# Performance work log

Measured on AMD Instinct MI355X. Metric: run time of the kernel, lower is better.

Reference implementation:

```python
import jax, jax.numpy as jnp
import numpy as np

NP_, NT_, D_, E_, EP_, L_, R_ = 100000, 300000, 64, 2000000, 500000, 2, 2


def setup_inputs() -> dict:
    key = jax.random.key(0)
    ks = jax.random.split(key, 12)
    return {
        "emb_playlist": jax.random.normal(ks[0], (NP_, D_), jnp.float32),
        "emb_track": jax.random.normal(ks[1], (NT_, D_), jnp.float32),
        "W_rel": jax.random.normal(ks[2], (L_, R_, D_, D_), jnp.float32) * 0.1,
        "W_root": jax.random.normal(ks[3], (L_, D_, D_), jnp.float32) * 0.1,
        "bias": jnp.zeros((L_, D_), jnp.float32),
        "n_id_playlist": jnp.arange(NP_, dtype=jnp.int32),
        "n_id_track": jnp.arange(NT_, dtype=jnp.int32),
        "edge_pt_src": jax.random.randint(ks[4], (E_,), 0, NP_, jnp.int32),
        "edge_pt_dst": jax.random.randint(ks[5], (E_,), 0, NT_, jnp.int32),
        "edge_tp_src": jax.random.randint(ks[6], (E_,), 0, NT_, jnp.int32),
        "edge_tp_dst": jax.random.randint(ks[7], (E_,), 0, NP_, jnp.int32),
        "ell_pl": jax.random.randint(ks[8], (EP_,), 0, NP_, jnp.int32),
        "ell_tr": jax.random.randint(ks[9], (EP_,), 0, NT_, jnp.int32),
    }


def _hetero_gnn(emb_playlist, emb_track, W_rel, W_root, bias,
                n_id_playlist, n_id_track,
                edge_pt_src, edge_pt_dst, edge_tp_src, edge_tp_dst,
                ell_pl, ell_tr):
    NP = emb_playlist.shape[0]
    NT = emb_track.shape[0]
    L = W_root.shape[0]
    N = NP + NT

    # embedding lookup by n_id (identity here, but faithful gather)
    x_pl = emb_playlist[n_id_playlist]
    x_tr = emb_track[n_id_track]

    # alpha=None -> uniform 1/(L+1); buffer is softmaxed -> still uniform
    weights = jax.nn.softmax(jnp.full((L + 1,), 1.0 / (L + 1), jnp.float32))

    out_pl = x_pl * weights[0]
    out_tr = x_tr * weights[0]

    # homogeneous layout: playlists at [0, NP), tracks at [NP, NP+NT)
    x = jnp.concatenate([x_pl, x_tr], axis=0)
    rel_edges = [
        (edge_pt_src, edge_pt_dst + NP),   # playlist -> track
        (edge_tp_src + NP, edge_tp_dst),   # track -> playlist
    ]

    for i in range(L):
        # RGCNConv: root transform + per-relation mean aggregation
        h = x @ W_root[i] + bias[i]
        for r, (src, dst) in enumerate(rel_edges):
            hr = x @ W_rel[i, r]              # [N, D] transform-then-gather
            msg = hr[src]                     # [E, D]
            ssum = jax.ops.segment_sum(msg, dst, num_segments=N)
            cnt = jax.ops.segment_sum(jnp.ones_like(dst, dtype=x.dtype), dst,
                                      num_segments=N)
            h = h + ssum / jnp.maximum(cnt, 1.0)[:, None]
        x = jax.nn.relu(h)
        out_pl = out_pl + x[:NP] * weights[i + 1]
        out_tr = out_tr + x[NP:] * weights[i + 1]

    # global -> local mapping via searchsorted (faithful happy path)
    ps_idx = jnp.argsort(n_id_playlist)
    ps = n_id_playlist[ps_idx]
    pl_loc = ps_idx[jnp.clip(jnp.searchsorted(ps, ell_pl), 0, NP - 1)]
    ts_idx = jnp.argsort(n_id_track)
    ts = n_id_track[ts_idx]
    tr_loc = ts_idx[jnp.clip(jnp.searchsorted(ts, ell_tr), 0, NT - 1)]

    # dot-product link scores (dropout p=0.0 -> identity)
    return jnp.sum(out_pl[pl_loc] * out_tr[tr_loc], axis=-1)


def reference(emb_playlist, emb_track, W_rel, W_root, bias,
              n_id_playlist, n_id_track,
              edge_pt_src, edge_pt_dst, edge_tp_src, edge_tp_dst,
              ell_pl, ell_tr):
    return _hetero_gnn(emb_playlist, emb_track, W_rel, W_root, bias,
                       n_id_playlist, n_id_track,
                       edge_pt_src, edge_pt_dst, edge_tp_src, edge_tp_dst,
                       ell_pl, ell_tr)
```

## Files before the change

kernel.cpp:

```cpp
#include <hip/hip_runtime.h>
#include <stdint.h>

typedef __attribute__((ext_vector_type(8))) short bf16x8;
typedef __attribute__((ext_vector_type(4))) float f32x4;

#define BN 1024
#define BNSHIFT 10
#define MAXNB 512
#define PTI 8192
#define PTHREADS 1024
#define EPT (PTI / PTHREADS)
#define SL 16
#define SSH 15
#define BINS (BN * SL)

static __device__ __forceinline__ float b2f_lo(uint32_t w) {
  union { uint32_t u; float f; } c; c.u = w << 16; return c.f;
}
static __device__ __forceinline__ float b2f_hi(uint32_t w) {
  union { uint32_t u; float f; } c; c.u = w & 0xffff0000u; return c.f;
}
static __device__ __forceinline__ uint16_t f2b(float f) {
  union { float f; uint32_t u; } c; c.f = f;
  return (uint16_t)((c.u + 0x7fffu + ((c.u >> 16) & 1u)) >> 16);
}
static __device__ __forceinline__ void acc8(float* s, uint4 v) {
  s[0] += b2f_lo(v.x); s[1] += b2f_hi(v.x);
  s[2] += b2f_lo(v.y); s[3] += b2f_hi(v.y);
  s[4] += b2f_lo(v.z); s[5] += b2f_hi(v.z);
  s[6] += b2f_lo(v.w); s[7] += b2f_hi(v.w);
}

__global__ __launch_bounds__(256) void convert_kernel(
    const float* __restrict__ emb_pl, const float* __restrict__ emb_tr,
    uint16_t* __restrict__ xb, int NP, int N) {
  long g = (long)blockIdx.x * 256 + threadIdx.x;
  long base8 = g * 8;
  long total = (long)N * 64;
  if (base8 >= total) return;
  long plEnd = (long)NP * 64;
  const float* src = (base8 < plEnd) ? (emb_pl + base8) : (emb_tr + (base8 - plEnd));
  f32x4 a = *(const f32x4*)src;
  f32x4 b = *(const f32x4*)(src + 4);
  union { uint16_t h[8]; uint4 v; } o;
  o.h[0] = f2b(a.x); o.h[1] = f2b(a.y); o.h[2] = f2b(a.z); o.h[3] = f2b(a.w);
  o.h[4] = f2b(b.x); o.h[5] = f2b(b.y); o.h[6] = f2b(b.z); o.h[7] = f2b(b.w);
  *(uint4*)(xb + base8) = o.v;
}

__global__ __launch_bounds__(256) void bucket_hist_kernel(
    const int* __restrict__ pt_dst, const int* __restrict__ tp_dst,
    int* __restrict__ bucketCount, int E, int NP, int NB) {
  extern __shared__ int hist[];
  int t = threadIdx.x;
  for (int b = t; b < NB; b += 256) hist[b] = 0;
  __syncthreads();
  long total = 2L * E;
  long stride = (long)gridDim.x * 256;
  for (long e = (long)blockIdx.x * 256 + t; e < total; e += stride) {
    int dstG = (e < E) ? (NP + pt_dst[e]) : tp_dst[e - E];
    atomicAdd(&hist[dstG >> BNSHIFT], 1);
  }
  __syncthreads();
  for (int b = t; b < NB; b += 256) {
    int h = hist[b];
    if (h > 0) atomicAdd(&bucketCount[b], h);
  }
}

__global__ __launch_bounds__(1024) void bucket_scan_kernel(
    const int* __restrict__ bucketCount, int* __restrict__ bucketStart,
    int* __restrict__ gCursor, int NB) {
  __shared__ int s[1024];
  int t = threadIdx.x;
  int K = (NB + 1023) >> 10;
  int b0 = t * K;
  int local = 0;
  for (int j = 0; j < K; ++j) {
    int b = b0 + j;
    if (b < NB) local += bucketCount[b];
  }
  int acc = local;
  s[t] = local;
  __syncthreads();
  for (int off = 1; off < 1024; off <<= 1) {
    int u = (t >= off) ? s[t - off] : 0;
    __syncthreads();
    acc += u;
    s[t] = acc;
    __syncthreads();
  }
  int run = acc - local;
  for (int j = 0; j < K; ++j) {
    int b = b0 + j;
    if (b < NB) {
      bucketStart[b] = run;
      gCursor[b] = run;
      run += bucketCount[b];
    }
  }
}

__global__ __launch_bounds__(PTHREADS) void partition_kernel(
    const int* __restrict__ pt_src, const int* __restrict__ pt_dst,
    const int* __restrict__ tp_src, const int* __restrict__ tp_dst,
    int* __restrict__ gCursor, uint32_t* __restrict__ pk,
    int E, int NP, int NB) {
  __shared__ uint64_t buf[PTI];
  __shared__ int hist[MAXNB];
  __shared__ int lstart[MAXNB];
  __shared__ int gbase[MAXNB];
  __shared__ int cur[MAXNB];
  __shared__ int sc[PTHREADS];
  int t = threadIdx.x;
  long total = 2L * E;
  long e0 = (long)blockIdx.x * PTI;
  long rem = total - e0;
  int cnt = (rem < (long)PTI) ? (int)rem : PTI;

  for (int j = t; j < NB; j += PTHREADS) hist[j] = 0;
  __syncthreads();

  int bj[EPT];
  uint32_t pkj[EPT];
#pragma unroll
  for (int j = 0; j < EPT; ++j) {
    int i = j * PTHREADS + t;
    bj[j] = -1;
    if (i < cnt) {
      long e = e0 + i;
      int dstG, src;
      if (e < E) {
        dstG = NP + __builtin_nontemporal_load(&pt_dst[e]);
        src = __builtin_nontemporal_load(&pt_src[e]);
      } else {
        dstG = __builtin_nontemporal_load(&tp_dst[e - E]);
        src = NP + __builtin_nontemporal_load(&tp_src[e - E]);
      }
      int b = dstG >> BNSHIFT;
      bj[j] = b;
      pkj[j] = ((uint32_t)(dstG & (BN - 1)) << 20) | (uint32_t)src;
      atomicAdd(&hist[b], 1);
    }
  }
  __syncthreads();

  int h = (t < NB) ? hist[t] : 0;
  int acc = h;
  sc[t] = h;
  __syncthreads();
  for (int off = 1; off < PTHREADS; off <<= 1) {
    int u = (t >= off) ? sc[t - off] : 0;
    __syncthreads();
    acc += u;
    sc[t] = acc;
    __syncthreads();
  }
  if (t < NB) {
    int ls = acc - h;
    lstart[t] = ls;
    cur[t] = ls;
    gbase[t] = (h > 0) ? atomicAdd(&gCursor[t], h) : 0;
  }
  __syncthreads();

#pragma unroll
  for (int j = 0; j < EPT; ++j) {
    int b = bj[j];
    if (b >= 0) {
      int pos = atomicAdd(&cur[b], 1);
      int gpos = gbase[b] + (pos - lstart[b]);
      buf[pos] = ((uint64_t)(uint32_t)gpos << 32) | (uint64_t)pkj[j];
    }
  }
  __syncthreads();

  for (int i = t; i < cnt; i += PTHREADS) {
    uint64_t e = buf[i];
    pk[(uint32_t)(e >> 32)] = (uint32_t)e;
  }
}

__global__ __launch_bounds__(1024) void local_csr_kernel(
    const int* __restrict__ bucketStart, const int* __restrict__ bucketCount,
    const uint32_t* __restrict__ pk, int* __restrict__ rowptr,
    int* __restrict__ col, int N, int TEtotal) {
  __shared__ int hist[BINS];
  __shared__ int ssum[1024];
  int t = threadIdx.x;
  int b = blockIdx.x;
  for (int j = t; j < BINS; j += 1024) hist[j] = 0;
  __syncthreads();
  int beg = bucketStart[b], num = bucketCount[b];
  for (int i = t; i < num; i += 1024) {
    uint32_t w = pk[beg + i];
    int bin = (int)(((w >> 20) << 4) | ((w & 0xFFFFFu) >> SSH));
    atomicAdd(&hist[bin], 1);
  }
  __syncthreads();
  int b0 = t * 16;
  int local = 0;
#pragma unroll
  for (int j = 0; j < 16; ++j) local += hist[b0 + j];
  int acc = local;
  ssum[t] = local;
  __syncthreads();
  for (int off = 1; off < 1024; off <<= 1) {
    int u = (t >= off) ? ssum[t - off] : 0;
    __syncthreads();
    acc += u;
    ssum[t] = acc;
    __syncthreads();
  }
  int run = acc - local;
  int node0 = (b << BNSHIFT) + t;
  if (node0 < N) rowptr[node0] = beg + run;
#pragma unroll
  for (int j = 0; j < 16; ++j) {
    int h = hist[b0 + j];
    hist[b0 + j] = run;
    run += h;
  }
  __syncthreads();
  for (int i = t; i < num; i += 1024) {
    uint32_t w = pk[beg + i];
    int bin = (int)(((w >> 20) << 4) | ((w & 0xFFFFFu) >> SSH));
    int pos = atomicAdd(&hist[bin], 1);
    col[beg + pos] = (int)(w & 0xFFFFFu);
  }
  if (b == 0 && t == 0) rowptr[N] = TEtotal;
}

__global__ __launch_bounds__(256) void pull_kernel(
    const int* __restrict__ rowptr, const int* __restrict__ col,
    const uint16_t* __restrict__ base, uint16_t* __restrict__ agg, int N) {
  int node = blockIdx.x * 32 + (threadIdx.x >> 3);
  int c = threadIdx.x & 7;
  if (node >= N) return;
  int beg = rowptr[node], end = rowptr[node + 1];
  float s[8] = {0, 0, 0, 0, 0, 0, 0, 0};
  const uint16_t* bp = base + c * 8;
  int i = beg;
  for (; i + 4 <= end; i += 4) {
    int c0 = col[i], c1 = col[i + 1], c2 = col[i + 2], c3 = col[i + 3];
    uint4 v0 = *(const uint4*)(bp + (size_t)c0 * 64);
    uint4 v1 = *(const uint4*)(bp + (size_t)c1 * 64);
    uint4 v2 = *(const uint4*)(bp + (size_t)c2 * 64);
    uint4 v3 = *(const uint4*)(bp + (size_t)c3 * 64);
    acc8(s, v0); acc8(s, v1); acc8(s, v2); acc8(s, v3);
  }
  for (; i < end; ++i)
    acc8(s, *(const uint4*)(bp + (size_t)col[i] * 64));
  int deg = end - beg;
  float inv = 1.0f / (float)(deg > 1 ? deg : 1);
  union { uint16_t h[8]; uint4 v; } o;
#pragma unroll
  for (int j = 0; j < 8; ++j) o.h[j] = f2b(s[j] * inv);
  *(uint4*)(agg + (size_t)node * 64 + c * 8) = o.v;
}

template <bool FUSE>
__global__ __launch_bounds__(256) void transform_kernel(
    const uint16_t* __restrict__ xpl, const uint16_t* __restrict__ xtr,
    const uint16_t* __restrict__ agg,
    const float* __restrict__ Wroot,
    const float* __restrict__ WrelP, const float* __restrict__ WrelT,
    const float* __restrict__ biasrow,
    const float* __restrict__ embP, const float* __restrict__ embT,
    uint16_t* __restrict__ xout, int NP, int NT, int BP) {
  int wave = threadIdx.x >> 6;
  int lane = threadIdx.x & 63;
  int m = lane & 15, q = lane >> 4;

  int wl, nw, ntiles, nodeBase;
  const uint16_t* xbase;
  const float* Wrel;
  const float* embBase;
  if ((int)blockIdx.x < BP) {
    wl = blockIdx.x * 4 + wave; nw = BP * 4; ntiles = NP / 16;
    xbase = xpl; Wrel = WrelP; nodeBase = 0; embBase = embP;
  } else {
    wl = (blockIdx.x - BP) * 4 + wave; nw = (gridDim.x - BP) * 4; ntiles = NT / 16;
    xbase = xtr; Wrel = WrelT; nodeBase = NP; embBase = embT;
  }

  bf16x8 br[2][4], bl[2][4];
  for (int kc = 0; kc < 2; ++kc)
    for (int ct = 0; ct < 4; ++ct) {
      int n = 16 * ct + m;
      int k0 = 32 * kc + 8 * q;
      bf16x8 t0, t1;
      for (int i = 0; i < 8; ++i) {
        t0[i] = (short)f2b(Wroot[(size_t)(k0 + i) * 64 + n]);
        t1[i] = (short)f2b(Wrel[(size_t)(k0 + i) * 64 + n]);
      }
      br[kc][ct] = t0;
      bl[kc][ct] = t1;
    }
  float bv[4];
  for (int ct = 0; ct < 4; ++ct) bv[ct] = biasrow[16 * ct + m];

  for (int t = wl; t < ntiles; t += nw) {
    int rowLocal = t * 16 + m;
    int nodeG = nodeBase + rowLocal;
    const uint16_t* xrow = xbase + (size_t)rowLocal * 64;
    bf16x8 ax0 = *(const bf16x8*)(xrow + 8 * q);
    bf16x8 ax1 = *(const bf16x8*)(xrow + 32 + 8 * q);

    const uint16_t* arow = agg + (size_t)nodeG * 64;
    bf16x8 aa0 = *(const bf16x8*)(arow + 8 * q);
    bf16x8 aa1 = *(const bf16x8*)(arow + 32 + 8 * q);

    f32x4 acc[4];
#pragma unroll
    for (int ct = 0; ct < 4; ++ct) acc[ct] = (f32x4){bv[ct], bv[ct], bv[ct], bv[ct]};
#pragma unroll
    for (int ct = 0; ct < 4; ++ct) {
      acc[ct] = __builtin_amdgcn_mfma_f32_16x16x32_bf16(ax0, br[0][ct], acc[ct], 0, 0, 0);
      acc[ct] = __builtin_amdgcn_mfma_f32_16x16x32_bf16(ax1, br[1][ct], acc[ct], 0, 0, 0);
      acc[ct] = __builtin_amdgcn_mfma_f32_16x16x32_bf16(aa0, bl[0][ct], acc[ct], 0, 0, 0);
      acc[ct] = __builtin_amdgcn_mfma_f32_16x16x32_bf16(aa1, bl[1][ct], acc[ct], 0, 0, 0);
    }
    int nodeRow0 = nodeBase + t * 16;
    int localRow0 = t * 16;
#pragma unroll
    for (int ct = 0; ct < 4; ++ct)
#pragma unroll
      for (int r = 0; r < 4; ++r) {
        float v = acc[ct][r];
        v = v > 0.0f ? v : 0.0f;
        int colIdx = 16 * ct + m;
        size_t go = (size_t)(nodeRow0 + 4 * q + r) * 64 + colIdx;
        if (FUSE) {
          size_t lo = (size_t)(localRow0 + 4 * q + r) * 64 + colIdx;
          float e = embBase[lo];
          float x1f = b2f_lo((uint32_t)xbase[lo]);
          xout[go] = f2b(e + x1f + v);
        } else {
          xout[go] = f2b(v);
        }
      }
  }
}

__global__ void score_kernel(const int* __restrict__ ell_pl,
                             const int* __restrict__ ell_tr,
                             const uint16_t* __restrict__ S,
                             float* __restrict__ out, int EP, int NP) {
  long g = (long)blockIdx.x * blockDim.x + threadIdx.x;
  long pair = g >> 3;
  int c = (int)(g & 7);
  if (pair >= EP) return;
  int p = __builtin_nontemporal_load(&ell_pl[pair]);
  int t = __builtin_nontemporal_load(&ell_tr[pair]);
  uint4 vp = *(const uint4*)(S + (size_t)p * 64 + c * 8);
  uint4 vt = *(const uint4*)(S + (size_t)(NP + t) * 64 + c * 8);
  float partial = b2f_lo(vp.x) * b2f_lo(vt.x) + b2f_hi(vp.x) * b2f_hi(vt.x)
                + b2f_lo(vp.y) * b2f_lo(vt.y) + b2f_hi(vp.y) * b2f_hi(vt.y)
                + b2f_lo(vp.z) * b2f_lo(vt.z) + b2f_hi(vp.z) * b2f_hi(vt.z)
                + b2f_lo(vp.w) * b2f_lo(vt.w) + b2f_hi(vp.w) * b2f_hi(vt.w);
  partial += __shfl_xor(partial, 1);
  partial += __shfl_xor(partial, 2);
  partial += __shfl_xor(partial, 4);
  if (c == 0) __builtin_nontemporal_store(partial * (1.0f / 9.0f), &out[pair]);
}

extern "C" void kernel_launch(void* const* d_in, const int* in_sizes, int n_in,
                              void* d_out, int out_size, void* d_ws, size_t ws_size,
                              hipStream_t stream) {
  const float* emb_pl = (const float*)d_in[0];
  const float* emb_tr = (const float*)d_in[1];
  const float* W_rel = (const float*)d_in[2];
  const float* W_root = (const float*)d_in[3];
  const float* bias = (const float*)d_in[4];
  const int* pt_src = (const int*)d_in[7];
  const int* pt_dst = (const int*)d_in[8];
  const int* tp_src = (const int*)d_in[9];
  const int* tp_dst = (const int*)d_in[10];
  const int* ell_pl = (const int*)d_in[11];
  const int* ell_tr = (const int*)d_in[12];
  float* out = (float*)d_out;

  const int NP = in_sizes[5];
  const int NT = in_sizes[6];
  const int E = in_sizes[7];
  const int EP = in_sizes[11];
  const int N = NP + NT;
  const long TE = 2L * E;
  const int NB = (N + BN - 1) / BN;

  char* ws = (char*)d_ws;
  size_t off = 0;
  uint16_t* agg = (uint16_t*)(ws + off); off += (size_t)N * 64 * 2;
  uint16_t* x1  = (uint16_t*)(ws + off); off += (size_t)N * 64 * 2;
  uint16_t* xb0 = (uint16_t*)(ws + off); off += (size_t)N * 64 * 2;
  uint16_t* S   = (uint16_t*)(ws + off); off += (size_t)N * 64 * 2;
  uint32_t* pk  = (uint32_t*)(ws + off); off += (size_t)TE * 4;
  int* col      = (int*)(ws + off);      off += (size_t)TE * 4;
  int* rowptr   = (int*)(ws + off);      off += (size_t)(N + 1) * 4;
  int* bucketCount = (int*)(ws + off);   off += (size_t)NB * 4;
  int* bucketStart = (int*)(ws + off);   off += (size_t)NB * 4;
  int* gCursor     = (int*)(ws + off);   off += (size_t)NB * 4;

  const int TB = 256;
  long cvt = ((long)N * 64 / 8 + TB - 1) / TB;
  int pullBlocks = (N + 31) / 32;
  int scoreBlocks = (int)(((long)EP * 8 + TB - 1) / TB);
  int partBlocks = (int)((TE + PTI - 1) / PTI);
  const int BP = 256, GT = 1024;

  convert_kernel<<<(int)cvt, TB, 0, stream>>>(emb_pl, emb_tr, xb0, NP, N);

  hipMemsetAsync(bucketCount, 0, (size_t)NB * 4, stream);
  bucket_hist_kernel<<<128, TB, NB * 4, stream>>>(pt_dst, tp_dst, bucketCount,
                                                  E, NP, NB);
  bucket_scan_kernel<<<1, 1024, 0, stream>>>(bucketCount, bucketStart, gCursor, NB);
  partition_kernel<<<partBlocks, PTHREADS, 0, stream>>>(
      pt_src, pt_dst, tp_src, tp_dst, gCursor, pk, E, NP, NB);
  local_csr_kernel<<<NB, 1024, 0, stream>>>(bucketStart, bucketCount, pk,
                                            rowptr, col, N, (int)TE);

  pull_kernel<<<pullBlocks, TB, 0, stream>>>(rowptr, col, xb0, agg, N);
  transform_kernel<false><<<GT, TB, 0, stream>>>(
      xb0, xb0 + (size_t)NP * 64, agg, W_root + 0 * 4096, W_rel + 1 * 4096,
      W_rel + 0 * 4096, bias + 0, nullptr, nullptr, x1, NP, NT, BP);

  pull_kernel<<<pullBlocks, TB, 0, stream>>>(rowptr, col, x1, agg, N);
  transform_kernel<true><<<GT, TB, 0, stream>>>(
      x1, x1 + (size_t)NP * 64, agg, W_root + 1 * 4096, W_rel + 3 * 4096,
      W_rel + 2 * 4096, bias + 64, emb_pl, emb_tr, S, NP, NT, BP);

  score_kernel<<<scoreBlocks, TB, 0, stream>>>(ell_pl, ell_tr, S, out, EP, NP);
}
```

Measured before the change: 536.4 us.

## Fuse convert with histogram kernel and stage transform output through LDS

Merges the fp32-to-bf16 embedding conversion and the destination-bucket histogram into one launch, splitting the grid by block index so both run concurrently and one launch is saved. In the transform kernel, MFMA results are staged through a per-wave shared-memory tile. Each lane then writes 16-byte vectorized rows and reads the residual embedding and x1 rows with vector loads, replacing scattered 2-byte stores and scalar loads. This costs extra LDS (about 17KB per block) and may lower occupancy.

```diff
diff --git a/kernel.cpp b/kernel.cpp
--- a/kernel.cpp
+++ b/kernel.cpp
@@ -31,40 +31,42 @@
   s[6] += b2f_lo(v.w); s[7] += b2f_hi(v.w);
 }
 
-__global__ __launch_bounds__(256) void convert_kernel(
+__global__ __launch_bounds__(256) void convert_hist_kernel(
     const float* __restrict__ emb_pl, const float* __restrict__ emb_tr,
-    uint16_t* __restrict__ xb, int NP, int N) {
-  long g = (long)blockIdx.x * 256 + threadIdx.x;
-  long base8 = g * 8;
-  long total = (long)N * 64;
-  if (base8 >= total) return;
-  long plEnd = (long)NP * 64;
-  const float* src = (base8 < plEnd) ? (emb_pl + base8) : (emb_tr + (base8 - plEnd));
-  f32x4 a = *(const f32x4*)src;
-  f32x4 b = *(const f32x4*)(src + 4);
-  union { uint16_t h[8]; uint4 v; } o;
-  o.h[0] = f2b(a.x); o.h[1] = f2b(a.y); o.h[2] = f2b(a.z); o.h[3] = f2b(a.w);
-  o.h[4] = f2b(b.x); o.h[5] = f2b(b.y); o.h[6] = f2b(b.z); o.h[7] = f2b(b.w);
-  *(uint4*)(xb + base8) = o.v;
-}
-
-__global__ __launch_bounds__(256) void bucket_hist_kernel(
+    uint16_t* __restrict__ xb,
     const int* __restrict__ pt_dst, const int* __restrict__ tp_dst,
-    int* __restrict__ bucketCount, int E, int NP, int NB) {
-  extern __shared__ int hist[];
+    int* __restrict__ bucketCount,
+    int NP, int N, int E, int NB, int cvtBlocks) {
+  __shared__ int hist[MAXNB];
   int t = threadIdx.x;
-  for (int b = t; b < NB; b += 256) hist[b] = 0;
-  __syncthreads();
-  long total = 2L * E;
-  long stride = (long)gridDim.x * 256;
-  for (long e = (long)blockIdx.x * 256 + t; e < total; e += stride) {
-    int dstG = (e < E) ? (NP + pt_dst[e]) : tp_dst[e - E];
-    atomicAdd(&hist[dstG >> BNSHIFT], 1);
-  }
-  __syncthreads();
-  for (int b = t; b < NB; b += 256) {
-    int h = hist[b];
-    if (h > 0) atomicAdd(&bucketCount[b], h);
+  if ((int)blockIdx.x < cvtBlocks) {
+    long g = (long)blockIdx.x * 256 + t;
+    long base8 = g * 8;
+    long total = (long)N * 64;
+    if (base8 >= total) return;
+    long plEnd = (long)NP * 64;
+    const float* src = (base8 < plEnd) ? (emb_pl + base8) : (emb_tr + (base8 - plEnd));
+    f32x4 a = *(const f32x4*)src;
+    f32x4 b = *(const f32x4*)(src + 4);
+    union { uint16_t h[8]; uint4 v; } o;
+    o.h[0] = f2b(a.x); o.h[1] = f2b(a.y); o.h[2] = f2b(a.z); o.h[3] = f2b(a.w);
+    o.h[4] = f2b(b.x); o.h[5] = f2b(b.y); o.h[6] = f2b(b.z); o.h[7] = f2b(b.w);
+    *(uint4*)(xb + base8) = o.v;
+  } else {
+    int hb = blockIdx.x - cvtBlocks;
+    for (int b = t; b < NB; b += 256) hist[b] = 0;
+    __syncthreads();
+    long total = 2L * E;
+    long stride = 128L * 256;
+    for (long e = (long)hb * 256 + t; e < total; e += stride) {
+      int dstG = (e < E) ? (NP + pt_dst[e]) : tp_dst[e - E];
+      atomicAdd(&hist[dstG >> BNSHIFT], 1);
+    }
+    __syncthreads();
+    for (int b = t; b < NB; b += 256) {
+      int h = hist[b];
+      if (h > 0) atomicAdd(&bucketCount[b], h);
+    }
   }
 }
 
@@ -268,9 +270,12 @@
     const float* __restrict__ biasrow,
     const float* __restrict__ embP, const float* __restrict__ embT,
     uint16_t* __restrict__ xout, int NP, int NT, int BP) {
+  __shared__ float tile[4][16][68];
   int wave = threadIdx.x >> 6;
   int lane = threadIdx.x & 63;
   int m = lane & 15, q = lane >> 4;
+  int g = lane >> 3, c = lane & 7;
+  float (*tp)[68] = tile[wave];
 
   int wl, nw, ntiles, nodeBase;
   const uint16_t* xbase;
@@ -321,25 +326,42 @@
       acc[ct] = __builtin_amdgcn_mfma_f32_16x16x32_bf16(aa0, bl[0][ct], acc[ct], 0, 0, 0);
       acc[ct] = __builtin_amdgcn_mfma_f32_16x16x32_bf16(aa1, bl[1][ct], acc[ct], 0, 0, 0);
     }
-    int nodeRow0 = nodeBase + t * 16;
-    int localRow0 = t * 16;
 #pragma unroll
     for (int ct = 0; ct < 4; ++ct)
 #pragma unroll
       for (int r = 0; r < 4; ++r) {
         float v = acc[ct][r];
-        v = v > 0.0f ? v : 0.0f;
-        int colIdx = 16 * ct + m;
-        size_t go = (size_t)(nodeRow0 + 4 * q + r) * 64 + colIdx;
-        if (FUSE) {
-          size_t lo = (size_t)(localRow0 + 4 * q + r) * 64 + colIdx;
-          float e = embBase[lo];
-          float x1f = b2f_lo((uint32_t)xbase[lo]);
-          xout[go] = f2b(e + x1f + v);
-        } else {
-          xout[go] = f2b(v);
-        }
+        tp[4 * q + r][16 * ct + m] = v > 0.0f ? v : 0.0f;
       }
+    int localRow0 = t * 16;
+    int nodeRow0 = nodeBase + localRow0;
+#pragma unroll
+    for (int rr = 0; rr < 2; ++rr) {
+      int row = g + rr * 8;
+      f32x4 va = *(const f32x4*)&tp[row][8 * c];
+      f32x4 vb = *(const f32x4*)&tp[row][8 * c + 4];
+      union { uint16_t h[8]; uint4 v; } o;
+      if (FUSE) {
+        const float* erow = embBase + (size_t)(localRow0 + row) * 64 + 8 * c;
+        f32x4 ea = *(const f32x4*)erow;
+        f32x4 eb = *(const f32x4*)(erow + 4);
+        uint4 xv = *(const uint4*)(xbase + (size_t)(localRow0 + row) * 64 + 8 * c);
+        o.h[0] = f2b(ea.x + b2f_lo(xv.x) + va.x);
+        o.h[1] = f2b(ea.y + b2f_hi(xv.x) + va.y);
+        o.h[2] = f2b(ea.z + b2f_lo(xv.y) + va.z);
+        o.h[3] = f2b(ea.w + b2f_hi(xv.y) + va.w);
+        o.h[4] = f2b(eb.x + b2f_lo(xv.z) + vb.x);
+        o.h[5] = f2b(eb.y + b2f_hi(xv.z) + vb.y);
+        o.h[6] = f2b(eb.z + b2f_lo(xv.w) + vb.z);
+        o.h[7] = f2b(eb.w + b2f_hi(xv.w) + vb.w);
+      } else {
+        o.h[0] = f2b(va.x); o.h[1] = f2b(va.y);
+        o.h[2] = f2b(va.z); o.h[3] = f2b(va.w);
+        o.h[4] = f2b(vb.x); o.h[5] = f2b(vb.y);
+        o.h[6] = f2b(vb.z); o.h[7] = f2b(vb.w);
+      }
+      *(uint4*)(xout + (size_t)(nodeRow0 + row) * 64 + 8 * c) = o.v;
+    }
   }
 }
 
@@ -403,17 +425,16 @@
   int* gCursor     = (int*)(ws + off);   off += (size_t)NB * 4;
 
   const int TB = 256;
-  long cvt = ((long)N * 64 / 8 + TB - 1) / TB;
+  int cvtBlocks = (int)(((long)N * 64 / 8 + TB - 1) / TB);
   int pullBlocks = (N + 31) / 32;
   int scoreBlocks = (int)(((long)EP * 8 + TB - 1) / TB);
   int partBlocks = (int)((TE + PTI - 1) / PTI);
   const int BP = 256, GT = 1024;
 
-  convert_kernel<<<(int)cvt, TB, 0, stream>>>(emb_pl, emb_tr, xb0, NP, N);
-
   hipMemsetAsync(bucketCount, 0, (size_t)NB * 4, stream);
-  bucket_hist_kernel<<<128, TB, NB * 4, stream>>>(pt_dst, tp_dst, bucketCount,
-                                                  E, NP, NB);
+  convert_hist_kernel<<<cvtBlocks + 128, TB, 0, stream>>>(
+      emb_pl, emb_tr, xb0, pt_dst, tp_dst, bucketCount, NP, N, E, NB, cvtBlocks);
+
   bucket_scan_kernel<<<1, 1024, 0, stream>>>(bucketCount, bucketStart, gCursor, NB);
   partition_kernel<<<partBlocks, PTHREADS, 0, stream>>>(
       pt_src, pt_dst, tp_src, tp_dst, gCursor, pk, E, NP, NB);
```

Result: no change. 527.2 us (-1.7%).
